# Optimization experiments

Measured on AMD Instinct MI355X. Metric: run time of the kernel, lower is better.

## Reference

```python
import jax, jax.numpy as jnp
import numpy as np

V, E, H, S = 32000, 1024, 1024, 2048


def setup_inputs() -> dict:
    key = jax.random.key(0)
    ks = jax.random.split(key, 16)
    std = 0.02
    return {
        "encoder_out": jax.random.normal(ks[0], (S, E), jnp.float32),
        "word_input": jax.random.randint(ks[1], (1,), 0, V, jnp.int32),
        "last_context": jax.random.normal(ks[2], (1, H), jnp.float32),
        "h0": jnp.zeros((1, 1, H), jnp.float32),
        "c0": jnp.zeros((1, 1, H), jnp.float32),
        # learned parameters
        "emb": jax.random.normal(ks[3], (V, E), jnp.float32) * std,
        "W_ih": jax.random.normal(ks[4], (4 * H, E + H), jnp.float32) * std,
        "W_hh": jax.random.normal(ks[5], (4 * H, H), jnp.float32) * std,
        "b_ih": jnp.zeros((4 * H,), jnp.float32),
        "b_hh": jnp.zeros((4 * H,), jnp.float32),
        "W_attn": jax.random.normal(ks[6], (H, E + H), jnp.float32) * std,
        "b_attn": jnp.zeros((H,), jnp.float32),
        "v": jax.random.uniform(ks[7], (H,), jnp.float32) * 0.1,
        "W_ah": jax.random.normal(ks[8], (H, E + H), jnp.float32) * std,
        "b_ah": jnp.zeros((H,), jnp.float32),
        "W_out": jax.random.normal(ks[9], (V, H), jnp.float32) * std,
        "b_out": jnp.zeros((V,), jnp.float32),
    }


def reference(encoder_out, word_input, last_context, h0, c0,
              emb, W_ih, W_hh, b_ih, b_hh,
              W_attn, b_attn, v, W_ah, b_ah, W_out, b_out):
    # single decoder step, batch=1 (dropout in eval mode == identity)
    embedded = emb[word_input[0]]                       # [E]
    x = jnp.concatenate([last_context[0], embedded])    # [H+E] (context first, as in torch.cat)
    # LSTM cell (PyTorch gate order i, f, g, o)
    gates = W_ih @ x + b_ih + W_hh @ h0[0, 0] + b_hh    # [4H]
    i, f, g, o = jnp.split(gates, 4)
    c = jax.nn.sigmoid(f) * c0[0, 0] + jax.nn.sigmoid(i) * jnp.tanh(g)
    ht = jax.nn.sigmoid(o) * jnp.tanh(c)                # [H]
    # additive attention, vectorized over encoder steps.
    # original concatenates (ht, encoder_out[i]); split attn weight accordingly.
    Wa_h, Wa_e = W_attn[:, :H], W_attn[:, H:]
    scores = jnp.tanh(encoder_out @ Wa_e.T + (Wa_h @ ht + b_attn)) @ v  # [S]
    w = jax.nn.softmax(scores)                          # [S]
    context = w @ encoder_out                           # [E]
    ht_tilda = jnp.tanh(W_ah @ jnp.concatenate([context, ht]) + b_ah)  # [H]
    output = jax.nn.log_softmax(W_out @ ht_tilda + b_out)              # [V]
    return (output[None, :], (ht[None, None, :], c[None, None, :]),
            ht_tilda[None, :], w[None, :])
```

## Files before the change

kernel.cpp:

```cpp
#include <hip/hip_runtime.h>
#include <math.h>

#define V_ 32000
#define E_ 1024
#define H_ 1024
#define S_ 2048

typedef __attribute__((ext_vector_type(8))) short bf16x8;
typedef __attribute__((ext_vector_type(8))) unsigned short u16x8;
typedef __attribute__((ext_vector_type(4))) float f32x4;

typedef __attribute__((address_space(1))) const unsigned int gu32;
typedef __attribute__((address_space(3))) unsigned int lu32;

__device__ __forceinline__ float sigmoidf_(float x) { return 1.0f / (1.0f + expf(-x)); }

__device__ __forceinline__ unsigned short f2bf(float f) {
    unsigned int u = __builtin_bit_cast(unsigned int, f);
    unsigned int r = (u + 0x7fffu + ((u >> 16) & 1u)) >> 16;
    return (unsigned short)r;
}
__device__ __forceinline__ float bf2f(unsigned short u) {
    return __builtin_bit_cast(float, ((unsigned int)u) << 16);
}
__device__ __forceinline__ u16x8 pack8(float4 a, float4 b) {
    u16x8 p;
    p[0] = f2bf(a.x); p[1] = f2bf(a.y); p[2] = f2bf(a.z); p[3] = f2bf(a.w);
    p[4] = f2bf(b.x); p[5] = f2bf(b.y); p[6] = f2bf(b.z); p[7] = f2bf(b.w);
    return p;
}
__device__ __forceinline__ void gload16(const void* g, void* l) {
    __builtin_amdgcn_global_load_lds((gu32*)g, (lu32*)l, 16, 0, 0);
}

__global__ __launch_bounds__(256) void kA(
    const float* __restrict__ W_ih, const float* __restrict__ W_hh,
    const float* __restrict__ b_ih, const float* __restrict__ b_hh,
    const float* __restrict__ last_context, const float* __restrict__ emb,
    const int* __restrict__ word, const float* __restrict__ h0,
    const float* __restrict__ c0, const float* __restrict__ enc,
    const float* __restrict__ W_attn,
    float* __restrict__ out_ht, float* __restrict__ out_c,
    float* __restrict__ ws_ht, unsigned short* __restrict__ encb,
    unsigned short* __restrict__ wab, float* __restrict__ ws_ctx)
{
    int b = blockIdx.x, tid = threadIdx.x;
    int wave = tid >> 6, lane = tid & 63;
    if (b < 1024) {
        __shared__ float sbuf[4];
        int j = b;
        const float* embrow = emb + (size_t)word[0] * E_;
        int row = j + wave * H_;
        const float* wi = W_ih + (size_t)row * (E_ + H_);
        const float* wh = W_hh + (size_t)row * H_;
        float acc = 0.f;
        #pragma unroll
        for (int it = 0; it < 8; ++it) {
            int idx = (lane + it * 64) * 4;
            float4 wv = *(const float4*)(wi + idx);
            float4 xv = (idx < H_) ? *(const float4*)(last_context + idx)
                                   : *(const float4*)(embrow + (idx - H_));
            acc = fmaf(wv.x, xv.x, acc); acc = fmaf(wv.y, xv.y, acc);
            acc = fmaf(wv.z, xv.z, acc); acc = fmaf(wv.w, xv.w, acc);
        }
        #pragma unroll
        for (int it = 0; it < 4; ++it) {
            int idx = (lane + it * 64) * 4;
            float4 wv = *(const float4*)(wh + idx);
            float4 hv = *(const float4*)(h0 + idx);
            acc = fmaf(wv.x, hv.x, acc); acc = fmaf(wv.y, hv.y, acc);
            acc = fmaf(wv.z, hv.z, acc); acc = fmaf(wv.w, hv.w, acc);
        }
        #pragma unroll
        for (int m = 32; m; m >>= 1) acc += __shfl_down(acc, m, 64);
        if (lane == 0) sbuf[wave] = acc;
        __syncthreads();
        if (tid == 0) {
            float gi = sbuf[0] + b_ih[j]          + b_hh[j];
            float gf = sbuf[1] + b_ih[j + H_]     + b_hh[j + H_];
            float gg = sbuf[2] + b_ih[j + 2*H_]   + b_hh[j + 2*H_];
            float go = sbuf[3] + b_ih[j + 3*H_]   + b_hh[j + 3*H_];
            float c  = sigmoidf_(gf) * c0[j] + sigmoidf_(gi) * tanhf(gg);
            float ht = sigmoidf_(go) * tanhf(c);
            out_c[j]  = c;
            out_ht[j] = ht;
            ws_ht[j]  = ht;
        }
        if (b == 0) {
            ws_ctx[tid]       = 0.f;
            ws_ctx[tid + 256] = 0.f;
            ws_ctx[tid + 512] = 0.f;
            ws_ctx[tid + 768] = 0.f;
        }
    } else {
        int cid = (b - 1024) * 256 + tid;
        const int ENC_CH = (S_ * E_) / 8;
        #pragma unroll
        for (int i = 0; i < 3; ++i) {
            int idx = cid + i * 131072;
            const float* src;
            unsigned short* dst;
            if (idx < ENC_CH) {
                src = enc + (size_t)idx * 8;
                dst = encb + (size_t)idx * 8;
            } else {
                int w = idx - ENC_CH;
                int h = w >> 7, off = (w & 127) * 8;
                src = W_attn + (size_t)h * (E_ + H_) + H_ + off;
                dst = wab + (size_t)h * E_ + off;
            }
            float4 a = *(const float4*)src;
            float4 bq = *(const float4*)(src + 4);
            *(u16x8*)dst = pack8(a, bq);
        }
    }
}

__global__ __launch_bounds__(256) void kC(
    const float* __restrict__ W_attn, const float* __restrict__ b_attn,
    const float* __restrict__ ws_ht,
    const unsigned short* __restrict__ encb, const unsigned short* __restrict__ wab,
    const float* __restrict__ v, float* __restrict__ spart)
{
    __shared__ unsigned short As[64 * 64];
    __shared__ unsigned short Bs[64 * 64];
    __shared__ float qsh[64], vsh[64];
    int bx = blockIdx.x, by = blockIdx.y;
    int s0 = bx * 64, h0 = by * 64;
    int tid = threadIdx.x;
    int wave = tid >> 6, lane = tid & 63;

    #pragma unroll 1
    for (int i = 0; i < 16; ++i) {
        int r = h0 + wave * 16 + i;
        const float* rowp = W_attn + (size_t)r * (E_ + H_);
        float acc = 0.f;
        #pragma unroll
        for (int it = 0; it < 4; ++it) {
            int idx = (lane + it * 64) * 4;
            float4 wv = *(const float4*)(rowp + idx);
            float4 hv = *(const float4*)(ws_ht + idx);
            acc = fmaf(wv.x, hv.x, acc); acc = fmaf(wv.y, hv.y, acc);
            acc = fmaf(wv.z, hv.z, acc); acc = fmaf(wv.w, hv.w, acc);
        }
        #pragma unroll
        for (int m = 32; m; m >>= 1) acc += __shfl_down(acc, m, 64);
        if (lane == 0) qsh[wave * 16 + i] = acc + b_attn[r];
    }
    if (tid < 64) vsh[tid] = v[h0 + tid];

    int r0 = tid >> 3, p0 = tid & 7;
    int lc = (p0 ^ (r0 & 7)) * 8;
    const unsigned short* aS0 = encb + (size_t)(s0 + r0) * E_ + lc;
    const unsigned short* aS1 = encb + (size_t)(s0 + 32 + r0) * E_ + lc;
    const unsigned short* bS0 = wab  + (size_t)(h0 + r0) * E_ + lc;
    const unsigned short* bS1 = wab  + (size_t)(h0 + 32 + r0) * E_ + lc;

    int wr = (wave >> 1) * 32, wc = (wave & 1) * 32;
    int fc = lane & 15, g = lane >> 4;
    int aRow[2], bRow[2], pc[2];
    #pragma unroll
    for (int m = 0; m < 2; ++m) aRow[m] = (wr + m * 16 + fc) * 64;
    #pragma unroll
    for (int n = 0; n < 2; ++n) bRow[n] = (wc + n * 16 + fc) * 64;
    #pragma unroll
    for (int kk = 0; kk < 2; ++kk) pc[kk] = ((kk * 4 + g) ^ (fc & 7)) * 8;

    f32x4 acc[2][2];
    #pragma unroll
    for (int m = 0; m < 2; ++m)
        #pragma unroll
        for (int n = 0; n < 2; ++n)
            acc[m][n] = (f32x4){0.f, 0.f, 0.f, 0.f};

    for (int t = 0; t < 16; ++t) {
        int k0 = t * 64;
        gload16(aS0 + k0, As + tid * 8);
        gload16(aS1 + k0, As + (tid + 256) * 8);
        gload16(bS0 + k0, Bs + tid * 8);
        gload16(bS1 + k0, Bs + (tid + 256) * 8);
        __syncthreads();
        #pragma unroll
        for (int kk = 0; kk < 2; ++kk) {
            bf16x8 af[2], bf2[2];
            #pragma unroll
            for (int m = 0; m < 2; ++m) af[m] = *(const bf16x8*)(As + aRow[m] + pc[kk]);
            #pragma unroll
            for (int n = 0; n < 2; ++n) bf2[n] = *(const bf16x8*)(Bs + bRow[n] + pc[kk]);
            #pragma unroll
            for (int m = 0; m < 2; ++m)
                #pragma unroll
                for (int n = 0; n < 2; ++n)
                    acc[m][n] = __builtin_amdgcn_mfma_f32_16x16x32_bf16(
                        af[m], bf2[n], acc[m][n], 0, 0, 0);
        }
        __syncthreads();
    }

    float qv[2], vv[2];
    #pragma unroll
    for (int n = 0; n < 2; ++n) {
        int col = wc + n * 16 + fc;
        qv[n] = qsh[col];
        vv[n] = vsh[col];
    }
    int part = by * 2 + (wave & 1);
    #pragma unroll
    for (int m = 0; m < 2; ++m) {
        #pragma unroll
        for (int j = 0; j < 4; ++j) {
            float p = 0.f;
            #pragma unroll
            for (int n = 0; n < 2; ++n)
                p += tanhf(acc[m][n][j] + qv[n]) * vv[n];
            #pragma unroll
            for (int mask = 8; mask; mask >>= 1) p += __shfl_xor(p, mask, 64);
            if (fc == 0)
                spart[(size_t)(s0 + wr + m * 16 + g * 4 + j) * 32 + part] = p;
        }
    }
}

__global__ __launch_bounds__(256) void kD(
    const float* __restrict__ spart, const unsigned short* __restrict__ encb,
    float* __restrict__ expw, float* __restrict__ gpart, float* __restrict__ ctx)
{
    __shared__ float esh[16];
    int b = blockIdx.x, tid = threadIdx.x;
    int s0 = b * 16;
    int sl = tid >> 4, pp = tid & 15;
    float vsum = spart[(size_t)(s0 + sl) * 32 + pp]
               + spart[(size_t)(s0 + sl) * 32 + pp + 16];
    #pragma unroll
    for (int mask = 8; mask; mask >>= 1) vsum += __shfl_xor(vsum, mask, 64);
    if (pp == 0) {
        float e = expf(vsum);
        expw[s0 + sl] = e;
        esh[sl] = e;
    }
    __syncthreads();
    if (tid == 0) {
        float bs = 0.f;
        #pragma unroll
        for (int i = 0; i < 16; ++i) bs += esh[i];
        gpart[b] = bs;
    }
    int e0 = tid * 4;
    float a0 = 0.f, a1 = 0.f, a2 = 0.f, a3 = 0.f;
    #pragma unroll
    for (int ss = 0; ss < 16; ++ss) {
        ushort4 u = *(const ushort4*)(encb + (size_t)(s0 + ss) * E_ + e0);
        float w = esh[ss];
        a0 = fmaf(w, bf2f(u.x), a0);
        a1 = fmaf(w, bf2f(u.y), a1);
        a2 = fmaf(w, bf2f(u.z), a2);
        a3 = fmaf(w, bf2f(u.w), a3);
    }
    atomicAdd(&ctx[e0 + 0], a0);
    atomicAdd(&ctx[e0 + 1], a1);
    atomicAdd(&ctx[e0 + 2], a2);
    atomicAdd(&ctx[e0 + 3], a3);
}

__global__ __launch_bounds__(64) void kE(
    const float* __restrict__ W_ah, const float* __restrict__ b_ah,
    const float* __restrict__ ctx, const float* __restrict__ ht,
    const float* __restrict__ gpart, const float* __restrict__ expw,
    float* __restrict__ out_htt, float* __restrict__ ws_htt,
    float* __restrict__ out_w)
{
    int b = blockIdx.x;
    int lane = threadIdx.x;
    float gsum = gpart[lane] + gpart[lane + 64];
    #pragma unroll
    for (int m = 32; m; m >>= 1) gsum += __shfl_xor(gsum, m, 64);
    float invS = 1.0f / gsum;
    if (b >= 1024) {
        int s = (b - 1024) * 256 + lane * 4;
        float4 e4 = *(const float4*)(expw + s);
        float4 w4 = { e4.x * invS, e4.y * invS, e4.z * invS, e4.w * invS };
        *(float4*)(out_w + s) = w4;
        return;
    }
    const float* row = W_ah + (size_t)b * (E_ + H_);
    float acc = 0.f;
    #pragma unroll
    for (int it = 0; it < 8; ++it) {
        int idx = (lane + it * 64) * 4;
        float4 wv = *(const float4*)(row + idx);
        float4 xv;
        if (idx < E_) {
            float4 cv = *(const float4*)(ctx + idx);
            xv = (float4){ cv.x * invS, cv.y * invS, cv.z * invS, cv.w * invS };
        } else {
            xv = *(const float4*)(ht + idx - E_);
        }
        acc = fmaf(wv.x, xv.x, acc); acc = fmaf(wv.y, xv.y, acc);
        acc = fmaf(wv.z, xv.z, acc); acc = fmaf(wv.w, xv.w, acc);
    }
    #pragma unroll
    for (int m = 32; m; m >>= 1) acc += __shfl_down(acc, m, 64);
    if (lane == 0) {
        float val = tanhf(acc + b_ah[b]);
        out_htt[b] = val;
        ws_htt[b]  = val;
    }
}

__global__ __launch_bounds__(256) void kF(
    const float* __restrict__ W_out, const float* __restrict__ b_out,
    const float* __restrict__ ht_tilda, float* __restrict__ logits,
    float* __restrict__ lpart)
{
    __shared__ float wes[4];
    int b = blockIdx.x;
    int wave = threadIdx.x >> 6, lane = threadIdx.x & 63;
    int r0 = b * 8 + wave * 2;
    const float* w0 = W_out + (size_t)r0 * H_;
    const float* w1 = W_out + (size_t)(r0 + 1) * H_;
    float a0 = 0.f, a1 = 0.f;
    #pragma unroll
    for (int it = 0; it < 4; ++it) {
        int idx = (lane + it * 64) * 4;
        float4 hv = *(const float4*)(ht_tilda + idx);
        float4 v0 = *(const float4*)(w0 + idx);
        float4 v1 = *(const float4*)(w1 + idx);
        a0 = fmaf(v0.x, hv.x, a0); a0 = fmaf(v0.y, hv.y, a0);
        a0 = fmaf(v0.z, hv.z, a0); a0 = fmaf(v0.w, hv.w, a0);
        a1 = fmaf(v1.x, hv.x, a1); a1 = fmaf(v1.y, hv.y, a1);
        a1 = fmaf(v1.z, hv.z, a1); a1 = fmaf(v1.w, hv.w, a1);
    }
    #pragma unroll
    for (int m = 32; m; m >>= 1) {
        a0 += __shfl_down(a0, m, 64);
        a1 += __shfl_down(a1, m, 64);
    }
    if (lane == 0) {
        float lg0 = a0 + b_out[r0];
        float lg1 = a1 + b_out[r0 + 1];
        logits[r0]     = lg0;
        logits[r0 + 1] = lg1;
        wes[wave] = expf(lg0) + expf(lg1);
    }
    __syncthreads();
    if (threadIdx.x == 0)
        lpart[b] = wes[0] + wes[1] + wes[2] + wes[3];
}

__global__ __launch_bounds__(1024) void kG(
    float* __restrict__ out, const float* __restrict__ lpart)
{
    __shared__ float sred[16];
    int b = blockIdx.x, tid = threadIdx.x;
    float s = 0.f;
    #pragma unroll
    for (int k = 0; k < 4; ++k) {
        int i = tid + k * 1024;
        if (i < 4000) s += lpart[i];
    }
    #pragma unroll
    for (int m = 32; m; m >>= 1) s += __shfl_down(s, m, 64);
    if ((tid & 63) == 0) sred[tid >> 6] = s;
    __syncthreads();
    float tot = 0.f;
    #pragma unroll
    for (int i = 0; i < 16; ++i) tot += sred[i];
    float lse = logf(tot);
    #pragma unroll
    for (int k = 0; k < 4; ++k) {
        int row = b * 4000 + k * 1024 + tid;
        if (row < (b + 1) * 4000 && row < V_) out[row] -= lse;
    }
}

extern "C" void kernel_launch(void* const* d_in, const int* in_sizes, int n_in,
                              void* d_out, int out_size, void* d_ws, size_t ws_size,
                              hipStream_t stream) {
    const float* enc          = (const float*)d_in[0];
    const int*   word         = (const int*)  d_in[1];
    const float* last_context = (const float*)d_in[2];
    const float* h0           = (const float*)d_in[3];
    const float* c0           = (const float*)d_in[4];
    const float* emb          = (const float*)d_in[5];
    const float* W_ih         = (const float*)d_in[6];
    const float* W_hh         = (const float*)d_in[7];
    const float* b_ih         = (const float*)d_in[8];
    const float* b_hh         = (const float*)d_in[9];
    const float* W_attn       = (const float*)d_in[10];
    const float* b_attn       = (const float*)d_in[11];
    const float* v            = (const float*)d_in[12];
    const float* W_ah         = (const float*)d_in[13];
    const float* b_ah         = (const float*)d_in[14];
    const float* W_out        = (const float*)d_in[15];
    const float* b_out        = (const float*)d_in[16];

    float* out        = (float*)d_out;
    float* out_logits = out;
    float* out_ht     = out + V_;
    float* out_c      = out + V_ + H_;
    float* out_htt    = out + V_ + 2 * H_;
    float* out_w      = out + V_ + 3 * H_;

    float* ws      = (float*)d_ws;
    float* ws_ht   = ws;
    float* ws_expw = ws + 1024;
    float* ws_ctx  = ws + 3072;
    float* ws_gp   = ws + 4096;
    float* ws_htt  = ws + 4224;
    float* ws_lp   = ws + 5248;
    float* ws_sp   = ws + 16384;
    unsigned short* encb = (unsigned short*)(ws + 81920);
    unsigned short* wab  = encb + (size_t)S_ * E_;

    kA<<<1536, 256, 0, stream>>>(W_ih, W_hh, b_ih, b_hh, last_context, emb, word,
                                 h0, c0, enc, W_attn, out_ht, out_c, ws_ht,
                                 encb, wab, ws_ctx);
    kC<<<dim3(32, 16), 256, 0, stream>>>(W_attn, b_attn, ws_ht, encb, wab, v, ws_sp);
    kD<<<128, 256, 0, stream>>>(ws_sp, encb, ws_expw, ws_gp, ws_ctx);
    kE<<<1032, 64, 0, stream>>>(W_ah, b_ah, ws_ctx, ws_ht, ws_gp, ws_expw,
                                out_htt, ws_htt, out_w);
    kF<<<4000, 256, 0, stream>>>(W_out, b_out, ws_htt, out_logits, ws_lp);
    kG<<<8, 1024, 0, stream>>>(out_logits, ws_lp);
}
```

Before: 84.87 us.

## Use nontemporal weight loads, overlap attention query GEMV with tile loads, regroup rows

Measured after the change: 92.41 us. 8.9% more time.

```diff
diff --git a/kernel.cpp b/kernel.cpp
--- a/kernel.cpp
+++ b/kernel.cpp
@@ -23,14 +23,17 @@
 __device__ __forceinline__ float bf2f(unsigned short u) {
     return __builtin_bit_cast(float, ((unsigned int)u) << 16);
 }
-__device__ __forceinline__ u16x8 pack8(float4 a, float4 b) {
+__device__ __forceinline__ u16x8 pack8(f32x4 a, f32x4 b) {
     u16x8 p;
-    p[0] = f2bf(a.x); p[1] = f2bf(a.y); p[2] = f2bf(a.z); p[3] = f2bf(a.w);
-    p[4] = f2bf(b.x); p[5] = f2bf(b.y); p[6] = f2bf(b.z); p[7] = f2bf(b.w);
+    p[0] = f2bf(a[0]); p[1] = f2bf(a[1]); p[2] = f2bf(a[2]); p[3] = f2bf(a[3]);
+    p[4] = f2bf(b[0]); p[5] = f2bf(b[1]); p[6] = f2bf(b[2]); p[7] = f2bf(b[3]);
     return p;
 }
 __device__ __forceinline__ void gload16(const void* g, void* l) {
     __builtin_amdgcn_global_load_lds((gu32*)g, (lu32*)l, 16, 0, 0);
+}
+__device__ __forceinline__ f32x4 ntload4(const float* p) {
+    return __builtin_nontemporal_load((const f32x4*)p);
 }
 
 __global__ __launch_bounds__(256) void kA(
@@ -57,19 +60,19 @@
         #pragma unroll
         for (int it = 0; it < 8; ++it) {
             int idx = (lane + it * 64) * 4;
-            float4 wv = *(const float4*)(wi + idx);
+            f32x4 wv = ntload4(wi + idx);
             float4 xv = (idx < H_) ? *(const float4*)(last_context + idx)
                                    : *(const float4*)(embrow + (idx - H_));
-            acc = fmaf(wv.x, xv.x, acc); acc = fmaf(wv.y, xv.y, acc);
-            acc = fmaf(wv.z, xv.z, acc); acc = fmaf(wv.w, xv.w, acc);
+            acc = fmaf(wv[0], xv.x, acc); acc = fmaf(wv[1], xv.y, acc);
+            acc = fmaf(wv[2], xv.z, acc); acc = fmaf(wv[3], xv.w, acc);
         }
         #pragma unroll
         for (int it = 0; it < 4; ++it) {
             int idx = (lane + it * 64) * 4;
-            float4 wv = *(const float4*)(wh + idx);
+            f32x4 wv = ntload4(wh + idx);
             float4 hv = *(const float4*)(h0 + idx);
-            acc = fmaf(wv.x, hv.x, acc); acc = fmaf(wv.y, hv.y, acc);
-            acc = fmaf(wv.z, hv.z, acc); acc = fmaf(wv.w, hv.w, acc);
+            acc = fmaf(wv[0], hv.x, acc); acc = fmaf(wv[1], hv.y, acc);
+            acc = fmaf(wv[2], hv.z, acc); acc = fmaf(wv[3], hv.w, acc);
         }
         #pragma unroll
         for (int m = 32; m; m >>= 1) acc += __shfl_down(acc, m, 64);
@@ -109,8 +112,8 @@
                 src = W_attn + (size_t)h * (E_ + H_) + H_ + off;
                 dst = wab + (size_t)h * E_ + off;
             }
-            float4 a = *(const float4*)src;
-            float4 bq = *(const float4*)(src + 4);
+            f32x4 a = ntload4(src);
+            f32x4 bq = ntload4(src + 4);
             *(u16x8*)dst = pack8(a, bq);
         }
     }
@@ -130,23 +133,6 @@
     int tid = threadIdx.x;
     int wave = tid >> 6, lane = tid & 63;
 
-    #pragma unroll 1
-    for (int i = 0; i < 16; ++i) {
-        int r = h0 + wave * 16 + i;
-        const float* rowp = W_attn + (size_t)r * (E_ + H_);
-        float acc = 0.f;
-        #pragma unroll
-        for (int it = 0; it < 4; ++it) {
-            int idx = (lane + it * 64) * 4;
-            float4 wv = *(const float4*)(rowp + idx);
-            float4 hv = *(const float4*)(ws_ht + idx);
-            acc = fmaf(wv.x, hv.x, acc); acc = fmaf(wv.y, hv.y, acc);
-            acc = fmaf(wv.z, hv.z, acc); acc = fmaf(wv.w, hv.w, acc);
-        }
-        #pragma unroll
-        for (int m = 32; m; m >>= 1) acc += __shfl_down(acc, m, 64);
-        if (lane == 0) qsh[wave * 16 + i] = acc + b_attn[r];
-    }
     if (tid < 64) vsh[tid] = v[h0 + tid];
 
     int r0 = tid >> 3, p0 = tid & 7;
@@ -173,12 +159,13 @@
         for (int n = 0; n < 2; ++n)
             acc[m][n] = (f32x4){0.f, 0.f, 0.f, 0.f};
 
+    gload16(aS0, As + tid * 8);
+    gload16(aS1, As + (tid + 256) * 8);
+    gload16(bS0, Bs + tid * 8);
+    gload16(bS1, Bs + (tid + 256) * 8);
+
+    #pragma unroll 1
     for (int t = 0; t < 16; ++t) {
-        int k0 = t * 64;
-        gload16(aS0 + k0, As + tid * 8);
-        gload16(aS1 + k0, As + (tid + 256) * 8);
-        gload16(bS0 + k0, Bs + tid * 8);
-        gload16(bS1 + k0, Bs + (tid + 256) * 8);
         __syncthreads();
         #pragma unroll
         for (int kk = 0; kk < 2; ++kk) {
@@ -194,7 +181,30 @@
                     acc[m][n] = __builtin_amdgcn_mfma_f32_16x16x32_bf16(
                         af[m], bf2[n], acc[m][n], 0, 0, 0);
         }
+        {
+            int r = h0 + wave * 16 + t;
+            const float* rowp = W_attn + (size_t)r * (E_ + H_);
+            float qa = 0.f;
+            #pragma unroll
+            for (int it = 0; it < 4; ++it) {
+                int idx = (lane + it * 64) * 4;
+                float4 wv = *(const float4*)(rowp + idx);
+                float4 hv = *(const float4*)(ws_ht + idx);
+                qa = fmaf(wv.x, hv.x, qa); qa = fmaf(wv.y, hv.y, qa);
+                qa = fmaf(wv.z, hv.z, qa); qa = fmaf(wv.w, hv.w, qa);
+            }
+            #pragma unroll
+            for (int m = 32; m; m >>= 1) qa += __shfl_down(qa, m, 64);
+            if (lane == 0) qsh[wave * 16 + t] = qa + b_attn[r];
+        }
         __syncthreads();
+        if (t < 15) {
+            int k0 = (t + 1) * 64;
+            gload16(aS0 + k0, As + tid * 8);
+            gload16(aS1 + k0, As + (tid + 256) * 8);
+            gload16(bS0 + k0, Bs + tid * 8);
+            gload16(bS1 + k0, Bs + (tid + 256) * 8);
+        }
     }
 
     float qv[2], vv[2];
@@ -262,7 +272,7 @@
     atomicAdd(&ctx[e0 + 3], a3);
 }
 
-__global__ __launch_bounds__(64) void kE(
+__global__ __launch_bounds__(256) void kE(
     const float* __restrict__ W_ah, const float* __restrict__ b_ah,
     const float* __restrict__ ctx, const float* __restrict__ ht,
     const float* __restrict__ gpart, const float* __restrict__ expw,
@@ -270,24 +280,25 @@
     float* __restrict__ out_w)
 {
     int b = blockIdx.x;
-    int lane = threadIdx.x;
+    int wave = threadIdx.x >> 6, lane = threadIdx.x & 63;
     float gsum = gpart[lane] + gpart[lane + 64];
     #pragma unroll
     for (int m = 32; m; m >>= 1) gsum += __shfl_xor(gsum, m, 64);
     float invS = 1.0f / gsum;
-    if (b >= 1024) {
-        int s = (b - 1024) * 256 + lane * 4;
+    if (b >= 256) {
+        int s = (b - 256) * 1024 + (int)threadIdx.x * 4;
         float4 e4 = *(const float4*)(expw + s);
         float4 w4 = { e4.x * invS, e4.y * invS, e4.z * invS, e4.w * invS };
         *(float4*)(out_w + s) = w4;
         return;
     }
-    const float* row = W_ah + (size_t)b * (E_ + H_);
+    int r = b * 4 + wave;
+    const float* row = W_ah + (size_t)r * (E_ + H_);
     float acc = 0.f;
     #pragma unroll
     for (int it = 0; it < 8; ++it) {
         int idx = (lane + it * 64) * 4;
-        float4 wv = *(const float4*)(row + idx);
+        f32x4 wv = ntload4(row + idx);
         float4 xv;
         if (idx < E_) {
             float4 cv = *(const float4*)(ctx + idx);
@@ -295,15 +306,15 @@
         } else {
             xv = *(const float4*)(ht + idx - E_);
         }
-        acc = fmaf(wv.x, xv.x, acc); acc = fmaf(wv.y, xv.y, acc);
-        acc = fmaf(wv.z, xv.z, acc); acc = fmaf(wv.w, xv.w, acc);
+        acc = fmaf(wv[0], xv.x, acc); acc = fmaf(wv[1], xv.y, acc);
+        acc = fmaf(wv[2], xv.z, acc); acc = fmaf(wv[3], xv.w, acc);
     }
     #pragma unroll
     for (int m = 32; m; m >>= 1) acc += __shfl_down(acc, m, 64);
     if (lane == 0) {
-        float val = tanhf(acc + b_ah[b]);
-        out_htt[b] = val;
-        ws_htt[b]  = val;
+        float val = tanhf(acc + b_ah[r]);
+        out_htt[r] = val;
+        ws_htt[r]  = val;
     }
 }
 
@@ -315,32 +326,44 @@
     __shared__ float wes[4];
     int b = blockIdx.x;
     int wave = threadIdx.x >> 6, lane = threadIdx.x & 63;
-    int r0 = b * 8 + wave * 2;
+    int r0 = b * 16 + wave * 4;
     const float* w0 = W_out + (size_t)r0 * H_;
     const float* w1 = W_out + (size_t)(r0 + 1) * H_;
-    float a0 = 0.f, a1 = 0.f;
+    const float* w2 = W_out + (size_t)(r0 + 2) * H_;
+    const float* w3 = W_out + (size_t)(r0 + 3) * H_;
+    float a0 = 0.f, a1 = 0.f, a2 = 0.f, a3 = 0.f;
     #pragma unroll
     for (int it = 0; it < 4; ++it) {
         int idx = (lane + it * 64) * 4;
         float4 hv = *(const float4*)(ht_tilda + idx);
-        float4 v0 = *(const float4*)(w0 + idx);
-        float4 v1 = *(const float4*)(w1 + idx);
-        a0 = fmaf(v0.x, hv.x, a0); a0 = fmaf(v0.y, hv.y, a0);
-        a0 = fmaf(v0.z, hv.z, a0); a0 = fmaf(v0.w, hv.w, a0);
-        a1 = fmaf(v1.x, hv.x, a1); a1 = fmaf(v1.y, hv.y, a1);
-        a1 = fmaf(v1.z, hv.z, a1); a1 = fmaf(v1.w, hv.w, a1);
+        f32x4 v0 = ntload4(w0 + idx);
+        f32x4 v1 = ntload4(w1 + idx);
+        f32x4 v2 = ntload4(w2 + idx);
+        f32x4 v3 = ntload4(w3 + idx);
+        a0 = fmaf(v0[0], hv.x, a0); a0 = fmaf(v0[1], hv.y, a0);
+        a0 = fmaf(v0[2], hv.z, a0); a0 = fmaf(v0[3], hv.w, a0);
+        a1 = fmaf(v1[0], hv.x, a1); a1 = fmaf(v1[1], hv.y, a1);
+        a1 = fmaf(v1[2], hv.z, a1); a1 = fmaf(v1[3], hv.w, a1);
+        a2 = fmaf(v2[0], hv.x, a2); a2 = fmaf(v2[1], hv.y, a2);
+        a2 = fmaf(v2[2], hv.z, a2); a2 = fmaf(v2[3], hv.w, a2);
+        a3 = fmaf(v3[0], hv.x, a3); a3 = fmaf(v3[1], hv.y, a3);
+        a3 = fmaf(v3[2], hv.z, a3); a3 = fmaf(v3[3], hv.w, a3);
     }
     #pragma unroll
     for (int m = 32; m; m >>= 1) {
-        a0 += __shfl_down(a0, m, 64);
-        a1 += __shfl_down(a1, m, 64);
+        a0 += __shfl_down(a0, m, 64); a1 += __shfl_down(a1, m, 64);
+        a2 += __shfl_down(a2, m, 64); a3 += __shfl_down(a3, m, 64);
     }
     if (lane == 0) {
         float lg0 = a0 + b_out[r0];
         float lg1 = a1 + b_out[r0 + 1];
+        float lg2 = a2 + b_out[r0 + 2];
+        float lg3 = a3 + b_out[r0 + 3];
         logits[r0]     = lg0;
         logits[r0 + 1] = lg1;
-        wes[wave] = expf(lg0) + expf(lg1);
+        logits[r0 + 2] = lg2;
+        logits[r0 + 3] = lg3;
+        wes[wave] = expf(lg0) + expf(lg1) + expf(lg2) + expf(lg3);
     }
     __syncthreads();
     if (threadIdx.x == 0)
@@ -354,9 +377,9 @@
     int b = blockIdx.x, tid = threadIdx.x;
     float s = 0.f;
     #pragma unroll
-    for (int k = 0; k < 4; ++k) {
+    for (int k = 0; k < 2; ++k) {
         int i = tid + k * 1024;
-        if (i < 4000) s += lpart[i];
+        if (i < 2000) s += lpart[i];
     }
     #pragma unroll
     for (int m = 32; m; m >>= 1) s += __shfl_down(s, m, 64);
@@ -417,8 +440,8 @@
                                  encb, wab, ws_ctx);
     kC<<<dim3(32, 16), 256, 0, stream>>>(W_attn, b_attn, ws_ht, encb, wab, v, ws_sp);
     kD<<<128, 256, 0, stream>>>(ws_sp, encb, ws_expw, ws_gp, ws_ctx);
-    kE<<<1032, 64, 0, stream>>>(W_ah, b_ah, ws_ctx, ws_ht, ws_gp, ws_expw,
+    kE<<<258, 256, 0, stream>>>(W_ah, b_ah, ws_ctx, ws_ht, ws_gp, ws_expw,
                                 out_htt, ws_htt, out_w);
-    kF<<<4000, 256, 0, stream>>>(W_out, b_out, ws_htt, out_logits, ws_lp);
+    kF<<<2000, 256, 0, stream>>>(W_out, b_out, ws_htt, out_logits, ws_lp);
     kG<<<8, 1024, 0, stream>>>(out_logits, ws_lp);
 }
```
